# Performance work log

Measured on AMD Instinct MI355X. Metric: run time of the kernel, lower is better.

## Reference

```python
import jax, jax.numpy as jnp
import numpy as np

N_NODES = 50000
N_EDGES = 800000
N_GRAPHS = 1000
IN_CH = 78
HID = 128
EPS = 1e-5


def _mean_aggr(x, src, dst, n):
    # scatter-mean of source-node features onto destination nodes
    s = jax.ops.segment_sum(x[src], dst, num_segments=n)
    deg = jax.ops.segment_sum(jnp.ones((src.shape[0],), x.dtype), dst, num_segments=n)
    return s / jnp.maximum(deg, 1.0)[:, None]


def _sage(x, src, dst, W_n, b_n, W_r):
    # PyG SAGEConv (mean): lin_l(mean_j x_j) + lin_r(x_i); lin_l has bias
    agg = _mean_aggr(x, src, dst, x.shape[0])
    return agg @ W_n + b_n + x @ W_r


def _bn(x, gamma, beta):
    # training-mode BatchNorm1d over node dimension (biased variance)
    mu = jnp.mean(x, axis=0)
    var = jnp.mean((x - mu) ** 2, axis=0)
    return (x - mu) * jax.lax.rsqrt(var + EPS) * gamma + beta


def setup_inputs() -> dict:
    key = jax.random.key(0)
    ks = jax.random.split(key, 20)
    d = {}
    d["x"] = jax.random.normal(ks[0], (N_NODES, IN_CH), dtype=jnp.float32)
    d["edge_index"] = jax.random.randint(ks[1], (2, N_EDGES), 0, N_NODES, dtype=jnp.int64)
    d["batch"] = jnp.sort(jax.random.randint(ks[2], (N_NODES,), 0, N_GRAPHS, dtype=jnp.int64))
    dims = [(IN_CH, HID), (HID, HID), (HID, HID)]
    for i, (di, do) in enumerate(dims):
        d[f"W_n{i}"] = jax.random.normal(ks[3 + 4 * i], (di, do), dtype=jnp.float32) * 0.05
        d[f"b{i}"] = jnp.zeros((do,), dtype=jnp.float32)
        d[f"W_r{i}"] = jax.random.normal(ks[4 + 4 * i], (di, do), dtype=jnp.float32) * 0.05
        d[f"g{i}"] = jnp.ones((do,), dtype=jnp.float32)
        d[f"be{i}"] = jnp.zeros((do,), dtype=jnp.float32)
    d["Wh1"] = jax.random.normal(ks[16], (HID, HID // 2), dtype=jnp.float32) * 0.05
    d["bh1"] = jnp.zeros((HID // 2,), dtype=jnp.float32)
    d["Wh2"] = jax.random.normal(ks[17], (HID // 2, 1), dtype=jnp.float32) * 0.05
    d["bh2"] = jnp.zeros((1,), dtype=jnp.float32)
    return d


def reference(x, edge_index, batch,
              W_n0, b0, W_r0, g0, be0,
              W_n1, b1, W_r1, g1, be1,
              W_n2, b2, W_r2, g2, be2,
              Wh1, bh1, Wh2, bh2):
    src, dst = edge_index[0], edge_index[1]
    layers = [(W_n0, b0, W_r0, g0, be0), (W_n1, b1, W_r1, g1, be1), (W_n2, b2, W_r2, g2, be2)]
    h = x
    for W_n, b_n, W_r, gamma, beta in layers:
        h = jax.nn.relu(_bn(_sage(h, src, dst, W_n, b_n, W_r), gamma, beta))
    # global mean pool per graph: [N_GRAPHS, HID]
    s = jax.ops.segment_sum(h, batch, num_segments=N_GRAPHS)
    cnt = jax.ops.segment_sum(jnp.ones((h.shape[0],), h.dtype), batch, num_segments=N_GRAPHS)
    pooled = s / jnp.maximum(cnt, 1.0)[:, None]
    return jax.nn.relu(pooled @ Wh1 + bh1) @ Wh2 + bh2
```

## Files before the change

### kernel.cpp

```cpp
#include <hip/hip_runtime.h>
#include <hip/hip_bf16.h>
#include <math.h>

#define HID 128
#define NSB 128
#define NBLK_BIN 256
#define BINC_CAP 6144

typedef short short8 __attribute__((ext_vector_type(8)));
typedef float f32x4 __attribute__((ext_vector_type(4)));

__global__ void prep_kernel(const float* __restrict__ x, float* __restrict__ xp,
                            int* __restrict__ bcnt, int nbuck16,
                            const float* __restrict__ Wn0, const float* __restrict__ Wr0,
                            const float* __restrict__ Wn1, const float* __restrict__ Wr1,
                            const float* __restrict__ Wn2, const float* __restrict__ Wr2,
                            unsigned short* __restrict__ B0h, unsigned short* __restrict__ B0l,
                            unsigned short* __restrict__ B1h, unsigned short* __restrict__ B1l,
                            unsigned short* __restrict__ B2h, unsigned short* __restrict__ B2l,
                            int N, int K0, int K0pad) {
    int i = blockIdx.x * blockDim.x + threadIdx.x;
    if (i < nbuck16) bcnt[i] = 0;
    if (i < N * K0pad) {
        int row = i / K0pad;
        int c = i - row * K0pad;
        xp[i] = (c < K0) ? x[(size_t)row * K0 + c] : 0.f;
    }
    int n0 = 256 * K0pad, n1 = 256 * HID;
    if (i < n0 + 2 * n1) {
        const float *Wn, *Wr;
        unsigned short *bh, *bl;
        int K, idx;
        if (i < n0) { Wn = Wn0; Wr = Wr0; bh = B0h; bl = B0l; K = K0; idx = i; }
        else if (i < n0 + n1) { Wn = Wn1; Wr = Wr1; bh = B1h; bl = B1l; K = HID; idx = i - n0; }
        else { Wn = Wn2; Wr = Wr2; bh = B2h; bl = B2l; K = HID; idx = i - n0 - n1; }
        int j = idx & 7;
        int lane = (idx >> 3) & 63;
        int cb = (idx >> 9) & 15;
        int ks = idx >> 13;
        int k = ks * 32 + ((lane >> 4) & 3) * 8 + j;
        int ch = 16 * cb + (lane & 15);
        float v = 0.f;
        if (k < K) v = (ch < 128) ? Wn[k * 128 + ch] : Wr[k * 128 + (ch - 128)];
        __hip_bfloat16 h = __float2bfloat16(v);
        float hf = __bfloat162float(h);
        __hip_bfloat16 l = __float2bfloat16(v - hf);
        bh[idx] = *(unsigned short*)&h;
        bl[idx] = *(unsigned short*)&l;
    }
}


__global__ void binA_kernel(const int* __restrict__ dst, int* __restrict__ bcnt,
                            int ne, int nbuck, int shift) {
    __shared__ int hist[512];
    int t = threadIdx.x;
    for (int i = t; i < 512; i += 256) hist[i] = 0;
    __syncthreads();
    size_t beg = (size_t)ne * blockIdx.x / NBLK_BIN;
    size_t end = (size_t)ne * (blockIdx.x + 1) / NBLK_BIN;
    for (size_t e = beg + t; e < end; e += 256)
        atomicAdd(&hist[dst[e] >> shift], 1);
    __syncthreads();
    for (int b = t; b < nbuck; b += 256) {
        int h = hist[b];
        if (h) atomicAdd(&bcnt[b * 16], h);
    }
}

__global__ __launch_bounds__(512) void bucket_scan_kernel(const int* __restrict__ bcnt,
                                                          int* __restrict__ bbase,
                                                          int* __restrict__ bcur, int nbuck) {
    __shared__ int tmp[512];
    int t = threadIdx.x;
    int v = (t < nbuck) ? bcnt[t * 16] : 0;
    tmp[t] = v;
    __syncthreads();
    for (int off = 1; off < 512; off <<= 1) {
        int u = 0;
        if (t >= off) u = tmp[t - off];
        __syncthreads();
        if (t >= off) tmp[t] += u;
        __syncthreads();
    }
    if (t < nbuck) {
        int exc = tmp[t] - v;
        bbase[t] = exc;
        bcur[t * 16] = exc;
        if (t == nbuck - 1) bbase[nbuck] = tmp[t];
    }
}

__global__ void binB_kernel(const int* __restrict__ src, const int* __restrict__ dst,
                            int* __restrict__ bcur, uint2* __restrict__ ebuf,
                            int ne, int nbuck, int shift) {
    __shared__ int hist[512];
    __shared__ int base[512];
    int t = threadIdx.x;
    for (int i = t; i < 512; i += 256) hist[i] = 0;
    __syncthreads();
    size_t beg = (size_t)ne * blockIdx.x / NBLK_BIN;
    size_t end = (size_t)ne * (blockIdx.x + 1) / NBLK_BIN;
    for (size_t e = beg + t; e < end; e += 256)
        atomicAdd(&hist[dst[e] >> shift], 1);
    __syncthreads();
    for (int b = t; b < nbuck; b += 256) {
        int h = hist[b];
        if (h) base[b] = atomicAdd(&bcur[b * 16], h);
        hist[b] = 0;
    }
    __syncthreads();
    for (size_t e = beg + t; e < end; e += 256) {
        int d = dst[e];
        int bk = d >> shift;
        int r = atomicAdd(&hist[bk], 1);
        ebuf[base[bk] + r] = make_uint2((unsigned)src[e], (unsigned)d);
    }
}

__global__ __launch_bounds__(512) void binC_kernel(const uint2* __restrict__ ebuf,
                                                   const int* __restrict__ bbase,
                                                   int* __restrict__ counts,
                                                   int* __restrict__ offsets,
                                                   int* __restrict__ esrc,
                                                   int N, int shift) {
    __shared__ int cnt[512], tmp[512], cur[512];
    __shared__ int sout[BINC_CAP];
    int b = blockIdx.x;
    int t = threadIdx.x;
    int node0 = b << shift;
    int npb = 1 << shift;
    if (node0 + npb > N) npb = N - node0;
    int ebase = bbase[b];
    int eend = bbase[b + 1];
    int total = eend - ebase;
    cnt[t] = 0;
    __syncthreads();
    for (int e = ebase + t; e < eend; e += 512)
        atomicAdd(&cnt[ebuf[e].y - node0], 1);
    __syncthreads();
    int v = cnt[t];
    tmp[t] = v;
    __syncthreads();
    for (int off = 1; off < 512; off <<= 1) {
        int u = 0;
        if (t >= off) u = tmp[t - off];
        __syncthreads();
        if (t >= off) tmp[t] += u;
        __syncthreads();
    }
    int exc = tmp[t] - v;
    cur[t] = exc;
    if (t < npb) {
        counts[node0 + t] = v;
        offsets[node0 + t] = ebase + exc;
    }
    __syncthreads();
    if (total <= BINC_CAP) {
        for (int e = ebase + t; e < eend; e += 512) {
            uint2 p = ebuf[e];
            int r = atomicAdd(&cur[(int)p.y - node0], 1);
            sout[r] = (int)p.x;
        }
        __syncthreads();
        for (int k = t; k < total; k += 512)
            esrc[ebase + k] = sout[k];
    } else {
        for (int e = ebase + t; e < eend; e += 512) {
            uint2 p = ebuf[e];
            int r = atomicAdd(&cur[(int)p.y - node0], 1);
            esrc[ebase + r] = (int)p.x;
        }
    }
}

__global__ __launch_bounds__(256) void gemm_kernel(
    const float* __restrict__ A, int Kpad,
    const float* __restrict__ psum, const float* __restrict__ psumsq,
    const float* __restrict__ g, const float* __restrict__ be,
    const unsigned short* __restrict__ Bswh, const unsigned short* __restrict__ Bswl,
    unsigned short* __restrict__ U16, float* __restrict__ V, int N) {
    int tid = threadIdx.x;
    int lane = tid & 63;
    int w = tid >> 6;
    int q = lane >> 4;
    int m = lane & 15;
    int n0 = blockIdx.x * 64;
    int apply_bn = (psum != nullptr);
    int LSTRv = Kpad + 8;

    __shared__ float s_sc[HID], s_sh[HID];
    __shared__ unsigned short sA_h[64 * (HID + 8)], sA_l[64 * (HID + 8)];
    if (apply_bn) {
        if (tid < HID) {
            double S = 0.0, Q = 0.0;
            for (int b = 0; b < NSB; b++) {
                S += (double)psum[b * HID + tid];
                Q += (double)psumsq[b * HID + tid];
            }
            double mu = S / (double)N;
            double var = Q / (double)N - mu * mu;
            if (var < 0.0) var = 0.0;
            float rs = (float)(1.0 / sqrt(var + 1e-5));
            float sc = g[tid] * rs;
            s_sc[tid] = sc;
            s_sh[tid] = be[tid] - (float)mu * sc;
        }
        __syncthreads();
    }

    int total = 64 * Kpad;
    for (int idx = tid * 4; idx < total; idx += 1024) {
        int row = idx / Kpad;
        int col = idx - row * Kpad;
        int grow = n0 + row;
        if (grow >= N) grow = N - 1;
        float4 z = *(const float4*)(A + (size_t)grow * Kpad + col);
        float y[4] = {z.x, z.y, z.z, z.w};
        if (apply_bn) {
#pragma unroll
            for (int j = 0; j < 4; j++)
                y[j] = fmaxf(fmaf(y[j], s_sc[col + j], s_sh[col + j]), 0.f);
        }
        ushort4 h4, l4;
        unsigned short* ph = (unsigned short*)&h4;
        unsigned short* pl = (unsigned short*)&l4;
#pragma unroll
        for (int j = 0; j < 4; j++) {
            __hip_bfloat16 h = __float2bfloat16(y[j]);
            float hf = __bfloat162float(h);
            __hip_bfloat16 lo = __float2bfloat16(y[j] - hf);
            ph[j] = *(unsigned short*)&h;
            pl[j] = *(unsigned short*)&lo;
        }
        *(ushort4*)&sA_h[row * LSTRv + col] = h4;
        *(ushort4*)&sA_l[row * LSTRv + col] = l4;
    }
    __syncthreads();

    f32x4 acc[4][4];
#pragma unroll
    for (int r = 0; r < 4; r++)
#pragma unroll
        for (int c = 0; c < 4; c++) acc[r][c] = (f32x4){0.f, 0.f, 0.f, 0.f};

    int ksteps = Kpad >> 5;
    for (int ks = 0; ks < ksteps; ks++) {
        int ko = ks * 32 + q * 8;
        short8 ah[4], al[4], bh[4], bl[4];
#pragma unroll
        for (int r = 0; r < 4; r++) {
            int ao = (16 * r + m) * LSTRv + ko;
            ah[r] = __builtin_bit_cast(short8, *(uint4*)&sA_h[ao]);
            al[r] = __builtin_bit_cast(short8, *(uint4*)&sA_l[ao]);
        }
#pragma unroll
        for (int c = 0; c < 4; c++) {
            int cb = 4 * w + c;
            size_t off = ((size_t)(ks * 16 + cb) * 64 + lane) * 8;
            bh[c] = __builtin_bit_cast(short8, *(const uint4*)(Bswh + off));
            bl[c] = __builtin_bit_cast(short8, *(const uint4*)(Bswl + off));
        }
#pragma unroll
        for (int r = 0; r < 4; r++)
#pragma unroll
            for (int c = 0; c < 4; c++) {
                acc[r][c] = __builtin_amdgcn_mfma_f32_16x16x32_bf16(ah[r], bh[c], acc[r][c], 0, 0, 0);
                acc[r][c] = __builtin_amdgcn_mfma_f32_16x16x32_bf16(ah[r], bl[c], acc[r][c], 0, 0, 0);
                acc[r][c] = __builtin_amdgcn_mfma_f32_16x16x32_bf16(al[r], bh[c], acc[r][c], 0, 0, 0);
            }
    }
    int colbase = (w & 1) * 64;
    if (w < 2) {
#pragma unroll
        for (int r = 0; r < 4; r++)
#pragma unroll
            for (int c = 0; c < 4; c++) {
                int col = colbase + 16 * c + m;
#pragma unroll
                for (int i = 0; i < 4; i++) {
                    int row = n0 + 16 * r + 4 * q + i;
                    if (row < N) {
                        __hip_bfloat16 h = __float2bfloat16(acc[r][c][i]);
                        U16[(size_t)row * HID + col] = *(unsigned short*)&h;
                    }
                }
            }
    } else {
#pragma unroll
        for (int r = 0; r < 4; r++)
#pragma unroll
            for (int c = 0; c < 4; c++) {
                int col = colbase + 16 * c + m;
#pragma unroll
                for (int i = 0; i < 4; i++) {
                    int row = n0 + 16 * r + 4 * q + i;
                    if (row < N) V[(size_t)row * HID + col] = acc[r][c][i];
                }
            }
    }
}

__global__ __launch_bounds__(256) void agg_kernel(const unsigned short* __restrict__ U16,
                                                  const float* __restrict__ V,
                                                  const float* __restrict__ bias,
                                                  const int* __restrict__ counts,
                                                  const int* __restrict__ offsets,
                                                  const int* __restrict__ esrc,
                                                  float* __restrict__ Z, int N) {
    int grp = threadIdx.x >> 5;
    int l32 = threadIdx.x & 31;
    int n = blockIdx.x * 8 + grp;
    if (n >= N) return;
    int deg = counts[n];
    int st = offsets[n];
    int co = 4 * l32;

    auto cvt = [](uint2 raw) -> f32x4 {
        f32x4 v;
        v[0] = __uint_as_float(raw.x << 16);
        v[1] = __uint_as_float(raw.x & 0xffff0000u);
        v[2] = __uint_as_float(raw.y << 16);
        v[3] = __uint_as_float(raw.y & 0xffff0000u);
        return v;
    };

    f32x4 a0 = {0,0,0,0}, a1 = {0,0,0,0}, a2 = {0,0,0,0}, a3 = {0,0,0,0};
    f32x4 a4 = {0,0,0,0}, a5 = {0,0,0,0}, a6 = {0,0,0,0}, a7 = {0,0,0,0};
    int i = 0;
    for (; i + 7 < deg; i += 8) {
        int s0 = esrc[st + i + 0], s1 = esrc[st + i + 1];
        int s2 = esrc[st + i + 2], s3 = esrc[st + i + 3];
        int s4 = esrc[st + i + 4], s5 = esrc[st + i + 5];
        int s6 = esrc[st + i + 6], s7 = esrc[st + i + 7];
        uint2 r0 = *(const uint2*)(U16 + (size_t)s0 * HID + co);
        uint2 r1 = *(const uint2*)(U16 + (size_t)s1 * HID + co);
        uint2 r2 = *(const uint2*)(U16 + (size_t)s2 * HID + co);
        uint2 r3 = *(const uint2*)(U16 + (size_t)s3 * HID + co);
        uint2 r4 = *(const uint2*)(U16 + (size_t)s4 * HID + co);
        uint2 r5 = *(const uint2*)(U16 + (size_t)s5 * HID + co);
        uint2 r6 = *(const uint2*)(U16 + (size_t)s6 * HID + co);
        uint2 r7 = *(const uint2*)(U16 + (size_t)s7 * HID + co);
        a0 += cvt(r0); a1 += cvt(r1); a2 += cvt(r2); a3 += cvt(r3);
        a4 += cvt(r4); a5 += cvt(r5); a6 += cvt(r6); a7 += cvt(r7);
    }
    for (; i + 3 < deg; i += 4) {
        int s0 = esrc[st + i + 0], s1 = esrc[st + i + 1];
        int s2 = esrc[st + i + 2], s3 = esrc[st + i + 3];
        uint2 r0 = *(const uint2*)(U16 + (size_t)s0 * HID + co);
        uint2 r1 = *(const uint2*)(U16 + (size_t)s1 * HID + co);
        uint2 r2 = *(const uint2*)(U16 + (size_t)s2 * HID + co);
        uint2 r3 = *(const uint2*)(U16 + (size_t)s3 * HID + co);
        a0 += cvt(r0); a1 += cvt(r1); a2 += cvt(r2); a3 += cvt(r3);
    }
    for (; i < deg; i++) {
        uint2 r0 = *(const uint2*)(U16 + (size_t)esrc[st + i] * HID + co);
        a0 += cvt(r0);
    }
    f32x4 acc = ((a0 + a1) + (a2 + a3)) + ((a4 + a5) + (a6 + a7));
    float d = (float)(deg > 1 ? deg : 1);
    f32x4 vv = ((const f32x4*)V)[(size_t)n * 32 + l32];
    f32x4 bb = ((const f32x4*)bias)[l32];
    ((f32x4*)Z)[(size_t)n * 32 + l32] = acc / d + vv + bb;
}

__global__ __launch_bounds__(256) void stats_kernel(const float* __restrict__ Z,
                                                    float* __restrict__ psum,
                                                    float* __restrict__ psumsq, int N) {
    int t = threadIdx.x;
    int cq = t & 31;
    int rg = t >> 5;
    const f32x4* Z4 = (const f32x4*)Z;
    f32x4 s = {0,0,0,0}, q = {0,0,0,0};
    for (int n = blockIdx.x * 8 + rg; n < N; n += NSB * 8) {
        f32x4 z = Z4[(size_t)n * 32 + cq];
        s += z;
        q += z * z;
    }
    __shared__ f32x4 bs[256], bq[256];
    bs[t] = s;
    bq[t] = q;
    __syncthreads();
#pragma unroll
    for (int off = 4; off > 0; off >>= 1) {
        if (rg < off) {
            bs[t] += bs[t + off * 32];
            bq[t] += bq[t + off * 32];
        }
        __syncthreads();
    }
    if (rg == 0) {
        ((f32x4*)psum)[blockIdx.x * 32 + cq] = bs[t];
        ((f32x4*)psumsq)[blockIdx.x * 32 + cq] = bq[t];
    }
}

__global__ __launch_bounds__(128) void pool_head_kernel(const float* __restrict__ Z,
                                                        const float* __restrict__ psum,
                                                        const float* __restrict__ psumsq,
                                                        const float* __restrict__ g,
                                                        const float* __restrict__ be,
                                                        const int* __restrict__ batch,
                                                        const float* __restrict__ Wh1,
                                                        const float* __restrict__ bh1,
                                                        const float* __restrict__ Wh2,
                                                        const float* __restrict__ bh2,
                                                        float* __restrict__ out, int N) {
    int gph = blockIdx.x;
    __shared__ int bounds[2];
    __shared__ float p[128];
    int t = threadIdx.x;
    if (t < 2) {
        int target = gph + t;
        int lo = 0, hi = N;
        while (lo < hi) {
            int mid = (lo + hi) >> 1;
            if (batch[mid] < target) lo = mid + 1;
            else hi = mid;
        }
        bounds[t] = lo;
    }
    double S = 0.0, Q = 0.0;
    for (int b = 0; b < NSB; b++) {
        S += (double)psum[b * HID + t];
        Q += (double)psumsq[b * HID + t];
    }
    double mu = S / (double)N;
    double var = Q / (double)N - mu * mu;
    if (var < 0.0) var = 0.0;
    float rs = (float)(1.0 / sqrt(var + 1e-5));
    float sc = g[t] * rs;
    float sh = be[t] - (float)mu * sc;
    __syncthreads();
    int start = bounds[0], end = bounds[1];
    float s = 0.f;
    for (int n = start; n < end; n++)
        s += fmaxf(fmaf(Z[(size_t)n * HID + t], sc, sh), 0.f);
    p[t] = s / fmaxf((float)(end - start), 1.f);
    __syncthreads();
    if (t < 64) {
        float acc = bh1[t];
        for (int k = 0; k < 128; k++) acc = fmaf(p[k], Wh1[k * 64 + t], acc);
        acc = fmaxf(acc, 0.f);
        float prod = acc * Wh2[t];
        for (int off = 32; off > 0; off >>= 1) prod += __shfl_down(prod, off);
        if (t == 0) out[gph] = prod + bh2[0];
    }
}

extern "C" void kernel_launch(void* const* d_in, const int* in_sizes, int n_in,
                              void* d_out, int out_size, void* d_ws, size_t ws_size,
                              hipStream_t stream) {
    const float* x = (const float*)d_in[0];
    const int* ei = (const int*)d_in[1];
    const int* batch = (const int*)d_in[2];
    const float* Wn[3] = {(const float*)d_in[3], (const float*)d_in[8], (const float*)d_in[13]};
    const float* bb[3] = {(const float*)d_in[4], (const float*)d_in[9], (const float*)d_in[14]};
    const float* Wr[3] = {(const float*)d_in[5], (const float*)d_in[10], (const float*)d_in[15]};
    const float* gg[3] = {(const float*)d_in[6], (const float*)d_in[11], (const float*)d_in[16]};
    const float* be[3] = {(const float*)d_in[7], (const float*)d_in[12], (const float*)d_in[17]};
    const float* Wh1 = (const float*)d_in[18];
    const float* bh1 = (const float*)d_in[19];
    const float* Wh2 = (const float*)d_in[20];
    const float* bh2 = (const float*)d_in[21];
    float* out = (float*)d_out;

    const int N = in_sizes[2];
    const int NE = in_sizes[1] / 2;
    const int NG = out_size;
    const int K0 = in_sizes[0] / N;
    const int K0pad = ((K0 + 31) / 32) * 32;

    const int* src = ei;
    const int* dst = ei + NE;

    int shift = 7;
    int nbuck = (N + 127) >> 7;
    while (nbuck > 512) { shift++; nbuck = (N + (1 << shift) - 1) >> shift; }

    char* w = (char*)d_ws;
    auto alloc = [&](size_t bytes) -> void* {
        void* p = (void*)w;
        w += (bytes + 255) & ~(size_t)255;
        return p;
    };
    unsigned short* bufU16 = (unsigned short*)alloc((size_t)N * HID * 2);
    float* bufV = (float*)alloc((size_t)N * HID * 4);
    float* bufZ = (float*)alloc((size_t)N * HID * 4);
    float* xp = (float*)alloc((size_t)N * K0pad * 4);
    unsigned short* BTh[3];
    unsigned short* BTl[3];
    BTh[0] = (unsigned short*)alloc((size_t)256 * K0pad * 2);
    BTl[0] = (unsigned short*)alloc((size_t)256 * K0pad * 2);
    BTh[1] = (unsigned short*)alloc((size_t)256 * HID * 2);
    BTl[1] = (unsigned short*)alloc((size_t)256 * HID * 2);
    BTh[2] = (unsigned short*)alloc((size_t)256 * HID * 2);
    BTl[2] = (unsigned short*)alloc((size_t)256 * HID * 2);
    int* counts = (int*)alloc((size_t)N * 4);
    int* offsets = (int*)alloc((size_t)(N + 1) * 4);
    int* esrc = (int*)alloc((size_t)NE * 4);
    int* bcnt = (int*)alloc((size_t)512 * 16 * 4);
    int* bcur = (int*)alloc((size_t)512 * 16 * 4);
    int* bbase = (int*)alloc((size_t)(512 + 1) * 4);
    float* pstats = (float*)alloc((size_t)3 * 2 * NSB * HID * 4);
    uint2* ebuf = (uint2*)bufZ;
    (void)ws_size;
    (void)n_in;

    size_t prep_total = (size_t)N * K0pad;
    prep_kernel<<<(prep_total + 255) / 256, 256, 0, stream>>>(
        x, xp, bcnt, nbuck * 16, Wn[0], Wr[0], Wn[1], Wr[1], Wn[2], Wr[2],
        BTh[0], BTl[0], BTh[1], BTl[1], BTh[2], BTl[2], N, K0, K0pad);

    binA_kernel<<<NBLK_BIN, 256, 0, stream>>>(dst, bcnt, NE, nbuck, shift);
    bucket_scan_kernel<<<1, 512, 0, stream>>>(bcnt, bbase, bcur, nbuck);
    binB_kernel<<<NBLK_BIN, 256, 0, stream>>>(src, dst, bcur, ebuf, NE, nbuck, shift);
    binC_kernel<<<nbuck, 512, 0, stream>>>(ebuf, bbase, counts, offsets, esrc, N, shift);

    int gblocks = (N + 63) / 64;
    int ablocks = (N + 7) / 8;
    for (int l = 0; l < 3; l++) {
        const float* Ain = (l == 0) ? xp : bufZ;
        int Kpad = (l == 0) ? K0pad : HID;
        const float* ppsum = (l == 0) ? (const float*)nullptr : pstats + (size_t)(l - 1) * 2 * NSB * HID;
        const float* ppsq = (l == 0) ? (const float*)nullptr : pstats + (size_t)(l - 1) * 2 * NSB * HID + NSB * HID;
        const float* pg = (l == 0) ? (const float*)nullptr : gg[l - 1];
        const float* pb = (l == 0) ? (const float*)nullptr : be[l - 1];
        gemm_kernel<<<gblocks, 256, 0, stream>>>(Ain, Kpad, ppsum, ppsq, pg, pb,
                                                 BTh[l], BTl[l], bufU16, bufV, N);
        agg_kernel<<<ablocks, 256, 0, stream>>>(bufU16, bufV, bb[l], counts, offsets, esrc, bufZ, N);
        stats_kernel<<<NSB, 256, 0, stream>>>(bufZ,
                                              pstats + (size_t)l * 2 * NSB * HID,
                                              pstats + (size_t)l * 2 * NSB * HID + NSB * HID, N);
    }

    pool_head_kernel<<<NG, 128, 0, stream>>>(bufZ,
                                             pstats + (size_t)2 * 2 * NSB * HID,
                                             pstats + (size_t)2 * 2 * NSB * HID + NSB * HID,
                                             gg[2], be[2], batch, Wh1, bh1, Wh2, bh2, out, N);
}
```

Before: 419.7 us.

## Template GEMM on padded K, halve row tile, batch A loads into registers

The GEMM kernel is templated on the padded K (96 or 128), which fully unrolls the k-loop and turns index divisions into constants. The row tile per block drops from 64 to 32, doubling the block count and halving shared memory per block for better occupancy. All A-tile global loads are issued into registers before conversion, so more memory requests are in flight. The trade-off is that each B fragment loaded from global memory is reused by fewer rows, raising B traffic per output.

```diff
diff --git a/kernel.cpp b/kernel.cpp
--- a/kernel.cpp
+++ b/kernel.cpp
@@ -50,7 +50,6 @@
     }
 }
 
-
 __global__ void binA_kernel(const int* __restrict__ dst, int* __restrict__ bcnt,
                             int ne, int nbuck, int shift) {
     __shared__ int hist[512];
@@ -174,23 +173,26 @@
     }
 }
 
+template <int KPAD>
 __global__ __launch_bounds__(256) void gemm_kernel(
-    const float* __restrict__ A, int Kpad,
+    const float* __restrict__ A,
     const float* __restrict__ psum, const float* __restrict__ psumsq,
     const float* __restrict__ g, const float* __restrict__ be,
     const unsigned short* __restrict__ Bswh, const unsigned short* __restrict__ Bswl,
     unsigned short* __restrict__ U16, float* __restrict__ V, int N) {
+    constexpr int LSTR = KPAD + 8;
+    constexpr int KSTEPS = KPAD / 32;
+    constexpr int ITERS = (32 * KPAD) / 1024;
     int tid = threadIdx.x;
     int lane = tid & 63;
     int w = tid >> 6;
     int q = lane >> 4;
     int m = lane & 15;
-    int n0 = blockIdx.x * 64;
+    int n0 = blockIdx.x * 32;
     int apply_bn = (psum != nullptr);
-    int LSTRv = Kpad + 8;
 
     __shared__ float s_sc[HID], s_sh[HID];
-    __shared__ unsigned short sA_h[64 * (HID + 8)], sA_l[64 * (HID + 8)];
+    __shared__ unsigned short sA_h[32 * LSTR], sA_l[32 * LSTR];
     if (apply_bn) {
         if (tid < HID) {
             double S = 0.0, Q = 0.0;
@@ -209,14 +211,22 @@
         __syncthreads();
     }
 
-    int total = 64 * Kpad;
-    for (int idx = tid * 4; idx < total; idx += 1024) {
-        int row = idx / Kpad;
-        int col = idx - row * Kpad;
+    float4 zreg[ITERS];
+#pragma unroll
+    for (int it = 0; it < ITERS; it++) {
+        int idx = tid * 4 + it * 1024;
+        int row = idx / KPAD;
+        int col = idx - row * KPAD;
         int grow = n0 + row;
         if (grow >= N) grow = N - 1;
-        float4 z = *(const float4*)(A + (size_t)grow * Kpad + col);
-        float y[4] = {z.x, z.y, z.z, z.w};
+        zreg[it] = *(const float4*)(A + (size_t)grow * KPAD + col);
+    }
+#pragma unroll
+    for (int it = 0; it < ITERS; it++) {
+        int idx = tid * 4 + it * 1024;
+        int row = idx / KPAD;
+        int col = idx - row * KPAD;
+        float y[4] = {zreg[it].x, zreg[it].y, zreg[it].z, zreg[it].w};
         if (apply_bn) {
 #pragma unroll
             for (int j = 0; j < 4; j++)
@@ -233,27 +243,21 @@
             ph[j] = *(unsigned short*)&h;
             pl[j] = *(unsigned short*)&lo;
         }
-        *(ushort4*)&sA_h[row * LSTRv + col] = h4;
-        *(ushort4*)&sA_l[row * LSTRv + col] = l4;
-    }
-    __syncthreads();
-
-    f32x4 acc[4][4];
-#pragma unroll
-    for (int r = 0; r < 4; r++)
+        *(ushort4*)&sA_h[row * LSTR + col] = h4;
+        *(ushort4*)&sA_l[row * LSTR + col] = l4;
+    }
+    __syncthreads();
+
+    f32x4 acc[2][4];
+#pragma unroll
+    for (int r = 0; r < 2; r++)
 #pragma unroll
         for (int c = 0; c < 4; c++) acc[r][c] = (f32x4){0.f, 0.f, 0.f, 0.f};
 
-    int ksteps = Kpad >> 5;
-    for (int ks = 0; ks < ksteps; ks++) {
+#pragma unroll
+    for (int ks = 0; ks < KSTEPS; ks++) {
         int ko = ks * 32 + q * 8;
-        short8 ah[4], al[4], bh[4], bl[4];
-#pragma unroll
-        for (int r = 0; r < 4; r++) {
-            int ao = (16 * r + m) * LSTRv + ko;
-            ah[r] = __builtin_bit_cast(short8, *(uint4*)&sA_h[ao]);
-            al[r] = __builtin_bit_cast(short8, *(uint4*)&sA_l[ao]);
-        }
+        short8 ah[2], al[2], bh[4], bl[4];
 #pragma unroll
         for (int c = 0; c < 4; c++) {
             int cb = 4 * w + c;
@@ -262,7 +266,13 @@
             bl[c] = __builtin_bit_cast(short8, *(const uint4*)(Bswl + off));
         }
 #pragma unroll
-        for (int r = 0; r < 4; r++)
+        for (int r = 0; r < 2; r++) {
+            int ao = (16 * r + m) * LSTR + ko;
+            ah[r] = __builtin_bit_cast(short8, *(uint4*)&sA_h[ao]);
+            al[r] = __builtin_bit_cast(short8, *(uint4*)&sA_l[ao]);
+        }
+#pragma unroll
+        for (int r = 0; r < 2; r++)
 #pragma unroll
             for (int c = 0; c < 4; c++) {
                 acc[r][c] = __builtin_amdgcn_mfma_f32_16x16x32_bf16(ah[r], bh[c], acc[r][c], 0, 0, 0);
@@ -273,7 +283,7 @@
     int colbase = (w & 1) * 64;
     if (w < 2) {
 #pragma unroll
-        for (int r = 0; r < 4; r++)
+        for (int r = 0; r < 2; r++)
 #pragma unroll
             for (int c = 0; c < 4; c++) {
                 int col = colbase + 16 * c + m;
@@ -288,7 +298,7 @@
             }
     } else {
 #pragma unroll
-        for (int r = 0; r < 4; r++)
+        for (int r = 0; r < 2; r++)
 #pragma unroll
             for (int c = 0; c < 4; c++) {
                 int col = colbase + 16 * c + m;
@@ -469,7 +479,7 @@
     const int NE = in_sizes[1] / 2;
     const int NG = out_size;
     const int K0 = in_sizes[0] / N;
-    const int K0pad = ((K0 + 31) / 32) * 32;
+    const int K0pad = (K0 <= 96) ? 96 : 128;
 
     const int* src = ei;
     const int* dst = ei + NE;
@@ -517,7 +527,7 @@
     binB_kernel<<<NBLK_BIN, 256, 0, stream>>>(src, dst, bcur, ebuf, NE, nbuck, shift);
     binC_kernel<<<nbuck, 512, 0, stream>>>(ebuf, bbase, counts, offsets, esrc, N, shift);
 
-    int gblocks = (N + 63) / 64;
+    int gblocks = (N + 31) / 32;
     int ablocks = (N + 7) / 8;
     for (int l = 0; l < 3; l++) {
         const float* Ain = (l == 0) ? xp : bufZ;
@@ -526,8 +536,12 @@
         const float* ppsq = (l == 0) ? (const float*)nullptr : pstats + (size_t)(l - 1) * 2 * NSB * HID + NSB * HID;
         const float* pg = (l == 0) ? (const float*)nullptr : gg[l - 1];
         const float* pb = (l == 0) ? (const float*)nullptr : be[l - 1];
-        gemm_kernel<<<gblocks, 256, 0, stream>>>(Ain, Kpad, ppsum, ppsq, pg, pb,
-                                                 BTh[l], BTl[l], bufU16, bufV, N);
+        if (Kpad == 96)
+            gemm_kernel<96><<<gblocks, 256, 0, stream>>>(Ain, ppsum, ppsq, pg, pb,
+                                                         BTh[l], BTl[l], bufU16, bufV, N);
+        else
+            gemm_kernel<128><<<gblocks, 256, 0, stream>>>(Ain, ppsum, ppsq, pg, pb,
+                                                          BTh[l], BTl[l], bufU16, bufV, N);
         agg_kernel<<<ablocks, 256, 0, stream>>>(bufU16, bufV, bb[l], counts, offsets, esrc, bufZ, N);
         stats_kernel<<<NSB, 256, 0, stream>>>(bufZ,
                                               pstats + (size_t)l * 2 * NSB * HID,
```

Result: faster. 401.8 us (-4.3%).
